# Kernel tuning notes

Measured on AMD Instinct MI355X. Metric: run time of the kernel, lower is better.

## Reference

```python
import jax, jax.numpy as jnp
import numpy as np

N, E, ND, ED, H, OUT, L, VC = 10000, 160000, 8, 4, 128, 256, 6, 6
HEADS, C = 4, 128  # GATConv: out_channels=128 per head, concat=False -> mean over heads


def _ln(x, g, b, eps=1e-5):
    m = x.mean(-1, keepdims=True)
    v = ((x - m) ** 2).mean(-1, keepdims=True)
    return (x - m) * jax.lax.rsqrt(v + eps) * g + b


def _gat_layer(h, src, dst, e_attr, lw, a_src, a_dst, lew, a_edge, bias):
    # h: [N,H]; e_attr: [Etot,H]; PyG GATConv(heads=4, concat=False, edge_dim=H)
    xh = (h @ lw).reshape(N, HEADS, C)                 # [N,4,128]
    eh = (e_attr @ lew).reshape(-1, HEADS, C)          # [Etot,4,128]
    al_s = jnp.einsum('nhc,hc->nh', xh, a_src)
    al_d = jnp.einsum('nhc,hc->nh', xh, a_dst)
    al_e = jnp.einsum('ehc,hc->eh', eh, a_edge)
    alpha = jax.nn.leaky_relu(al_s[src] + al_d[dst] + al_e, 0.2)  # [Etot,4]
    amax = jax.ops.segment_max(alpha, dst, num_segments=N)
    ex = jnp.exp(alpha - amax[dst])
    den = jax.ops.segment_sum(ex, dst, num_segments=N)
    w = ex / (den[dst] + 1e-16)
    out = jax.ops.segment_sum(xh[src] * w[..., None], dst, num_segments=N)  # [N,4,128]
    return out.mean(axis=1) + bias


def setup_inputs() -> dict:
    key = jax.random.key(0)
    ks = jax.random.split(key, 32)
    s = 0.05
    d = {
        'x': jax.random.normal(ks[0], (N, ND), jnp.float32),
        'edge_index': jax.random.randint(ks[1], (2, E), 0, N),
        'edge_attr': jax.random.uniform(ks[2], (E, ED), jnp.float32),
        'vnf_context': jax.random.normal(ks[3], (1, VC), jnp.float32),
        # node embedding
        'node_w': jax.random.normal(ks[4], (ND, H)) * s, 'node_b': jnp.zeros((H,)),
        # EdgeAttentionLayer
        'ea_proj_w': jax.random.normal(ks[5], (ED, H)) * s, 'ea_proj_b': jnp.zeros((H,)),
        'vnf_w': jax.random.normal(ks[6], (VC, H)) * s, 'vnf_b': jnp.zeros((H,)),
        'att1_w': jax.random.normal(ks[7], (2 * H, H)) * s, 'att1_b': jnp.zeros((H,)),
        'att2_w': jax.random.normal(ks[8], (H, H // 2)) * s, 'att2_b': jnp.zeros((H // 2,)),
        'att3_w': jax.random.normal(ks[9], (H // 2, 1)) * s, 'att3_b': jnp.zeros((1,)),
        # per-layer GATConv params (stacked over L layers)
        'gat_lin_w': jax.random.normal(ks[10], (L, H, HEADS * C)) * s,
        'gat_att_src': jax.random.normal(ks[11], (L, HEADS, C)) * s,
        'gat_att_dst': jax.random.normal(ks[12], (L, HEADS, C)) * s,
        'gat_lin_edge_w': jax.random.normal(ks[13], (L, H, HEADS * C)) * s,
        'gat_att_edge': jax.random.normal(ks[14], (L, HEADS, C)) * s,
        'gat_bias': jnp.zeros((L, C)),
        'ln_scale': jnp.ones((L, H)), 'ln_bias': jnp.zeros((L, H)),
        # output projection
        'out_w': jax.random.normal(ks[15], (H, OUT)) * s, 'out_b': jnp.zeros((OUT,)),
    }
    return d


def reference(x, edge_index, edge_attr, vnf_context, node_w, node_b, ea_proj_w, ea_proj_b,
              vnf_w, vnf_b, att1_w, att1_b, att2_w, att2_b, att3_w, att3_b,
              gat_lin_w, gat_att_src, gat_att_dst, gat_lin_edge_w, gat_att_edge, gat_bias,
              ln_scale, ln_bias, out_w, out_b):
    src, dst = edge_index[0], edge_index[1]
    h = x @ node_w + node_b                                   # [N,128]
    # EdgeAttentionLayer (eval mode, no network_state)
    ef = edge_attr @ ea_proj_w + ea_proj_b                    # [E,128]
    vnf = vnf_context @ vnf_w + vnf_b                         # [1,128]
    comb = jnp.concatenate([ef, jnp.broadcast_to(vnf, (E, H))], axis=-1)
    a = jax.nn.relu(comb @ att1_w + att1_b)
    a = jax.nn.relu(a @ att2_w + att2_b)
    e_gate = jax.nn.sigmoid(a @ att3_w + att3_b)              # [E,1]
    w_edge = ef * e_gate                                      # [E,128]
    # GATConv default add_self_loops=True, fill_value='mean'
    loop = jnp.arange(N)
    src2 = jnp.concatenate([src, loop])
    dst2 = jnp.concatenate([dst, loop])
    e2 = jnp.concatenate([w_edge, jnp.broadcast_to(w_edge.mean(0, keepdims=True), (N, H))], axis=0)
    for l in range(L):
        hc = _gat_layer(h, src2, dst2, e2, gat_lin_w[l], gat_att_src[l], gat_att_dst[l],
                        gat_lin_edge_w[l], gat_att_edge[l], gat_bias[l])
        h = _ln(h + jax.nn.relu(hc), ln_scale[l], ln_bias[l])
    return h @ out_w + out_b                                  # [N,256]
```

## Files before the change

### kernel.cpp

```cpp
#include <hip/hip_runtime.h>
#include <hip/hip_bf16.h>
#include <math.h>

#define Nn 10000
#define Ee 160000
#define LL 6

typedef short v8s __attribute__((ext_vector_type(8)));
typedef float v4f __attribute__((ext_vector_type(4)));

__device__ __forceinline__ unsigned short f2bf(float v) {
    unsigned int b = __float_as_uint(v);
    b += 0x7fffu + ((b >> 16) & 1u);
    return (unsigned short)(b >> 16);
}
__device__ __forceinline__ float bflo(unsigned int u) { return __uint_as_float(u << 16); }
__device__ __forceinline__ float bfhi(unsigned int u) { return __uint_as_float(u & 0xffff0000u); }

__global__ __launch_bounds__(256) void k_first(
    const float* __restrict__ x, const float* __restrict__ nw,
    const float* __restrict__ nb, float* __restrict__ h, unsigned short* __restrict__ hb,
    const int* __restrict__ ei, int* __restrict__ hist,
    const float* __restrict__ glw, const float* __restrict__ gas,
    const float* __restrict__ gad, const float* __restrict__ glew,
    const float* __restrict__ gae, float* __restrict__ Bs,
    float* __restrict__ Bd, float* __restrict__ Be,
    unsigned short* __restrict__ WsumT,
    const float* __restrict__ a2w, unsigned short* __restrict__ w2bf,
    const float* __restrict__ ow, unsigned short* __restrict__ owbT,
    const float* __restrict__ vnfc, const float* __restrict__ vw,
    const float* __restrict__ vb, const float* __restrict__ eab,
    const float* __restrict__ a1w, const float* __restrict__ a1b,
    const float* __restrict__ eaw, float* __restrict__ E1) {
    __shared__ float vr[128];
    __shared__ float sM1[512];
    __shared__ float sd1[128];
    int b = blockIdx.x, t = threadIdx.x;
    if (b < 5000) {
        int idx = b * 256 + t;
        int n = idx >> 7, c = idx & 127;
        const float* xr = x + (size_t)n * 8;
        float acc = nb[c];
#pragma unroll
        for (int k = 0; k < 8; k++) acc += xr[k] * nw[k * 128 + c];
        h[idx] = acc;
        hb[idx] = f2bf(acc);
        return;
    }
    if (b < 5625) {
        int i = (b - 5000) * 256 + t;
        atomicAdd(&hist[ei[Ee + i]], 1);
        return;
    }
    if (b < 5637) {
        int idx = (b - 5625) * 256 + t;
        if (idx >= LL * 128 * 4) return;
        int hh = idx & 3, k = (idx >> 2) & 127, l = idx >> 9;
        const float* lwp = glw  + (size_t)l * 65536 + k * 512 + hh * 128;
        const float* lep = glew + (size_t)l * 65536 + k * 512 + hh * 128;
        const float* sp = gas + l * 512 + hh * 128;
        const float* dp = gad + l * 512 + hh * 128;
        const float* ep = gae + l * 512 + hh * 128;
        float s1 = 0, s2 = 0, s3 = 0;
        for (int c = 0; c < 128; c++) {
            float lv = lwp[c];
            s1 += lv * sp[c];
            s2 += lv * dp[c];
            s3 += lep[c] * ep[c];
        }
        Bs[idx] = s1; Bd[idx] = s2; Be[idx] = s3;
        return;
    }
    if (b < 7173) {
        int idx = (b - 5637) * 256 + t;
        int kk = idx & 511;
        int c = (idx >> 9) & 127;
        int l = idx >> 16;
        float v = 0.25f * glw[(size_t)l * 65536 + (size_t)(kk & 127) * 512 + (kk >> 7) * 128 + c];
        WsumT[(size_t)l * 65536 + (size_t)c * 512 + kk] = f2bf(v);
        return;
    }
    if (b < 7205) {
        int idx = (b - 7173) * 256 + t;
        int j = idx & 7, lane = (idx >> 3) & 63, nt = (idx >> 9) & 3, ks = idx >> 11;
        int k = ks * 32 + ((lane >> 4) << 3) + j;
        int n = nt * 16 + (lane & 15);
        w2bf[idx] = f2bf(a2w[k * 64 + n]);
        return;
    }
    if (b < 7333) {
        int idx = (b - 7205) * 256 + t;
        int col = idx >> 7, kk = idx & 127;
        owbT[idx] = f2bf(ow[kk * 256 + col]);
        return;
    }
    {
        if (t < 128) {
            float a = vb[t];
#pragma unroll
            for (int k = 0; k < 6; k++) a += vnfc[k] * vw[k * 128 + t];
            vr[t] = a;
        }
        __syncthreads();
        if (t < 128) {
            float a = a1b[t];
            for (int k = 0; k < 128; k++) a += eab[k] * a1w[k * 128 + t];
            for (int k = 0; k < 128; k++) a += vr[k] * a1w[(128 + k) * 128 + t];
            sd1[t] = a;
        }
#pragma unroll
        for (int rr = 0; rr < 2; rr++) {
            int id = rr * 256 + t;
            int r = id >> 7, j = id & 127;
            float a = 0.f;
            for (int k = 0; k < 128; k++) a += eaw[r * 128 + k] * a1w[k * 128 + j];
            sM1[id] = a;
        }
        __syncthreads();
        if (t < 128) {
            E1[t * 8 + 0] = sM1[t];
            E1[t * 8 + 1] = sM1[128 + t];
            E1[t * 8 + 2] = sM1[256 + t];
            E1[t * 8 + 3] = sM1[384 + t];
            E1[t * 8 + 4] = sd1[t];
            E1[t * 8 + 5] = 0.f; E1[t * 8 + 6] = 0.f; E1[t * 8 + 7] = 0.f;
        }
    }
}

__global__ __launch_bounds__(1024) void k_scan(
    const int* __restrict__ hist, int* __restrict__ seg, int* __restrict__ pos,
    const float* __restrict__ eaw, const float* __restrict__ eab,
    const float* __restrict__ Be, float* __restrict__ PB, float* __restrict__ cB) {
    __shared__ int wsums[16];
    __shared__ int carry_s;
    int t = threadIdx.x;
    if (blockIdx.x == 1) {
        if (t >= 24) return;
        int l = t >> 2, hh = t & 3;
        const float* bp = Be + l * 512 + hh;
        float s0 = 0, s1 = 0, s2 = 0, s3 = 0, sc = 0;
        for (int k = 0; k < 128; k++) {
            float bv = bp[k * 4];
            s0 += eaw[0 * 128 + k] * bv;
            s1 += eaw[1 * 128 + k] * bv;
            s2 += eaw[2 * 128 + k] * bv;
            s3 += eaw[3 * 128 + k] * bv;
            sc += eab[k] * bv;
        }
        PB[0 * 24 + t] = s0; PB[1 * 24 + t] = s1;
        PB[2 * 24 + t] = s2; PB[3 * 24 + t] = s3;
        cB[t] = sc;
        return;
    }
    int lane = t & 63, wid = t >> 6;
    if (t == 0) { carry_s = 0; seg[0] = 0; }
    __syncthreads();
    for (int base = 0; base < Nn; base += 1024) {
        int idx = base + t;
        int v = (idx < Nn) ? hist[idx] : 0;
        int sc = v;
#pragma unroll
        for (int d = 1; d < 64; d <<= 1) {
            int up = __shfl_up(sc, d);
            if (lane >= d) sc += up;
        }
        if (lane == 63) wsums[wid] = sc;
        __syncthreads();
        if (wid == 0) {
            int wv = (lane < 16) ? wsums[lane] : 0;
            int wsc = wv;
#pragma unroll
            for (int d = 1; d < 16; d <<= 1) {
                int up = __shfl_up(wsc, d);
                if (lane >= d) wsc += up;
            }
            if (lane < 16) wsums[lane] = wsc - wv;
        }
        __syncthreads();
        int carry = carry_s;
        int inc = sc + wsums[wid] + carry;
        if (idx < Nn) { seg[idx + 1] = inc; pos[idx] = inc - v; }
        __syncthreads();
        if (t == 1023) carry_s = inc;
        __syncthreads();
    }
}

__global__ __launch_bounds__(256, 2) void k_edge(
    const float* __restrict__ ea, const float* __restrict__ E1,
    const unsigned short* __restrict__ w2bf,
    const float* __restrict__ a2b, const float* __restrict__ a3w,
    const float* __restrict__ a3b,
    const float* __restrict__ PB, const float* __restrict__ cB,
    const int* __restrict__ ei, int* __restrict__ pos, int* __restrict__ srcv,
    float* __restrict__ aleT, float* __restrict__ gsum,
    const float* __restrict__ h, const float* __restrict__ Bs,
    const float* __restrict__ Bd, float* __restrict__ als, float* __restrict__ ald) {
    __shared__ float4 sM[128];
    __shared__ float sD[128];
    __shared__ float4 sevs[256];
    __shared__ float gsh[256];
    __shared__ float sgsum[5];
    int t = threadIdx.x;
    int b = blockIdx.x;
    if (b >= 625) {
        int idx = (b - 625) * 256 + t;
        if (idx >= Nn * 8) return;
        int n = idx >> 3, slot = idx & 7;
        const float* B = (slot < 4) ? Bs : Bd;
        int hh = slot & 3;
        const float4* hr = (const float4*)(h + (size_t)n * 128);
        float s = 0.f;
#pragma unroll 8
        for (int kb = 0; kb < 32; kb++) {
            float4 hv = hr[kb];
            s += hv.x * B[(4 * kb + 0) * 4 + hh] + hv.y * B[(4 * kb + 1) * 4 + hh]
               + hv.z * B[(4 * kb + 2) * 4 + hh] + hv.w * B[(4 * kb + 3) * 4 + hh];
        }
        if (slot < 4) als[n * 4 + hh] = s;
        else          ald[n * 4 + hh] = s;
        return;
    }
    int lane = t & 63;
    int wid = t >> 6;
    int c = lane & 15, q = lane >> 4;
    int eb0 = b * 256;

    int my_src = ei[eb0 + t];
    int my_dst = ei[Ee + eb0 + t];
    sevs[t] = *(const float4*)(ea + (size_t)(eb0 + t) * 4);
    if (t < 128) {
        int slot = t ^ ((t >> 3) & 3);
        sM[slot] = *(const float4*)(E1 + t * 8);
        sD[t] = E1[t * 8 + 4];
    }
    if (t < 5) sgsum[t] = 0.f;
    __syncthreads();

    float4 ev4[4];
#pragma unroll
    for (int mt = 0; mt < 4; mt++) ev4[mt] = sevs[(wid * 4 + mt) * 16 + c];

    v8s av[4][4];
#pragma unroll
    for (int ks = 0; ks < 4; ks++) {
        float4 mr[8]; float dr[8];
#pragma unroll
        for (int j = 0; j < 8; j++) {
            int k = ks * 32 + q * 8 + j;
            mr[j] = sM[k ^ q];
            dr[j] = sD[k];
        }
#pragma unroll
        for (int mt = 0; mt < 4; mt++) {
            float4 ev = ev4[mt];
            v8s a;
#pragma unroll
            for (int j = 0; j < 8; j++) {
                float xv = fmaxf(dr[j] + ev.x * mr[j].x + ev.y * mr[j].y
                                       + ev.z * mr[j].z + ev.w * mr[j].w, 0.f);
                a[j] = (short)f2bf(xv);
            }
            av[mt][ks] = a;
        }
    }

    v4f acc[4][4];
#pragma unroll
    for (int nt = 0; nt < 4; nt++) {
        float bb = a2b[nt * 16 + c];
#pragma unroll
        for (int mt = 0; mt < 4; mt++) acc[mt][nt] = (v4f){bb, bb, bb, bb};
    }
#pragma unroll
    for (int nt = 0; nt < 4; nt++) {
#pragma unroll
        for (int ks = 0; ks < 4; ks++) {
            v8s bfr = *(const v8s*)(w2bf + ((size_t)(ks * 4 + nt) * 64 + lane) * 8);
#pragma unroll
            for (int mt = 0; mt < 4; mt++)
                acc[mt][nt] = __builtin_amdgcn_mfma_f32_16x16x32_bf16(av[mt][ks], bfr, acc[mt][nt], 0, 0, 0);
        }
    }

    float a3r[4];
#pragma unroll
    for (int nt = 0; nt < 4; nt++) a3r[nt] = a3w[nt * 16 + c];
    float a3b0 = a3b[0];
#pragma unroll
    for (int mt = 0; mt < 4; mt++) {
#pragma unroll
        for (int r = 0; r < 4; r++) {
            float s = 0.f;
#pragma unroll
            for (int nt = 0; nt < 4; nt++) s += fmaxf(acc[mt][nt][r], 0.f) * a3r[nt];
            s += __shfl_xor(s, 1); s += __shfl_xor(s, 2);
            s += __shfl_xor(s, 4); s += __shfl_xor(s, 8);
            if (c == 0) gsh[(wid * 4 + mt) * 16 + q * 4 + r] = 1.f / (1.f + __expf(-(s + a3b0)));
        }
    }
    __syncthreads();

    float g = gsh[t];
    float4 evv = sevs[t];
    float v0 = g, v1 = g * evv.x, v2 = g * evv.y, v3 = g * evv.z, v4 = g * evv.w;
#pragma unroll
    for (int d = 32; d > 0; d >>= 1) {
        v0 += __shfl_down(v0, d); v1 += __shfl_down(v1, d); v2 += __shfl_down(v2, d);
        v3 += __shfl_down(v3, d); v4 += __shfl_down(v4, d);
    }
    if (lane == 0) {
        atomicAdd(&sgsum[0], v0); atomicAdd(&sgsum[1], v1); atomicAdd(&sgsum[2], v2);
        atomicAdd(&sgsum[3], v3); atomicAdd(&sgsum[4], v4);
    }
    __syncthreads();
    if (t < 5) atomicAdd(&gsum[t], sgsum[t]);
    int slot = atomicAdd(&pos[my_dst], 1);
    srcv[slot] = my_src;
#pragma unroll
    for (int i4 = 0; i4 < 6; i4++) {
        float4 cc = *(const float4*)(cB + i4 * 4);
        float4 p0 = *(const float4*)(PB + 0 * 24 + i4 * 4);
        float4 p1 = *(const float4*)(PB + 1 * 24 + i4 * 4);
        float4 p2 = *(const float4*)(PB + 2 * 24 + i4 * 4);
        float4 p3 = *(const float4*)(PB + 3 * 24 + i4 * 4);
        float4 o;
        o.x = g * (cc.x + evv.x * p0.x + evv.y * p1.x + evv.z * p2.x + evv.w * p3.x);
        o.y = g * (cc.y + evv.x * p0.y + evv.y * p1.y + evv.z * p2.y + evv.w * p3.y);
        o.z = g * (cc.z + evv.x * p0.z + evv.y * p1.z + evv.z * p2.z + evv.w * p3.z);
        o.w = g * (cc.w + evv.x * p0.w + evv.y * p1.w + evv.z * p2.w + evv.w * p3.w);
        *(float4*)(aleT + (size_t)i4 * Ee * 4 + (size_t)slot * 4) = o;
    }
}

__global__ __launch_bounds__(256) void k_agg3(
    const int* __restrict__ srcv, const int* __restrict__ seg,
    const float* __restrict__ als, const float* __restrict__ ald,
    const float* __restrict__ aleS_l,
    const unsigned short* __restrict__ hb, unsigned short* __restrict__ aggb,
    const float* __restrict__ gsum, const float* __restrict__ PBl,
    const float* __restrict__ cBl) {
    __shared__ float part[2][512];
    __shared__ float pden[2][4];
    int t = threadIdx.x;
    int lane = t & 63;
    int wv = (t >> 6) & 1;
    int w = t >> 7;
    int n = blockIdx.x * 2 + w;
    int start = seg[n], end = seg[n + 1];
    int deg = end - start;
    int half = (deg + 1) >> 1;
    int s0 = start + wv * half;
    int e0 = wv ? end : start + half;
    int hp = lane >> 4;
    int cch = (lane & 15) * 8;
    float aldh = ald[n * 4 + hp];
    float den = 0.f;
    float4 acc0 = make_float4(0.f, 0.f, 0.f, 0.f);
    float4 acc1 = make_float4(0.f, 0.f, 0.f, 0.f);
    int i = s0;
    for (; i + 4 <= e0; i += 4) {
        int sa = srcv[i], sb = srcv[i + 1], sc = srcv[i + 2], sd = srcv[i + 3];
        float ala = aleS_l[(size_t)(i + 0) * 4 + hp];
        float alb = aleS_l[(size_t)(i + 1) * 4 + hp];
        float alc = aleS_l[(size_t)(i + 2) * 4 + hp];
        float ald_ = aleS_l[(size_t)(i + 3) * 4 + hp];
        float asa = als[sa * 4 + hp], asb = als[sb * 4 + hp];
        float asc = als[sc * 4 + hp], asd = als[sd * 4 + hp];
        uint4 ua = *(const uint4*)(hb + (size_t)sa * 128 + cch);
        uint4 ub = *(const uint4*)(hb + (size_t)sb * 128 + cch);
        uint4 uc = *(const uint4*)(hb + (size_t)sc * 128 + cch);
        uint4 ud = *(const uint4*)(hb + (size_t)sd * 128 + cch);
        float ava = asa + aldh + ala; ava = ava > 0.f ? ava : 0.2f * ava;
        float avb = asb + aldh + alb; avb = avb > 0.f ? avb : 0.2f * avb;
        float avc = asc + aldh + alc; avc = avc > 0.f ? avc : 0.2f * avc;
        float avd = asd + aldh + ald_; avd = avd > 0.f ? avd : 0.2f * avd;
        float ea = __expf(fminf(ava, 60.f));
        float eb = __expf(fminf(avb, 60.f));
        float ec = __expf(fminf(avc, 60.f));
        float ed = __expf(fminf(avd, 60.f));
        den += (ea + eb) + (ec + ed);
        acc0.x += (ea * bflo(ua.x) + eb * bflo(ub.x)) + (ec * bflo(uc.x) + ed * bflo(ud.x));
        acc0.y += (ea * bfhi(ua.x) + eb * bfhi(ub.x)) + (ec * bfhi(uc.x) + ed * bfhi(ud.x));
        acc0.z += (ea * bflo(ua.y) + eb * bflo(ub.y)) + (ec * bflo(uc.y) + ed * bflo(ud.y));
        acc0.w += (ea * bfhi(ua.y) + eb * bfhi(ub.y)) + (ec * bfhi(uc.y) + ed * bfhi(ud.y));
        acc1.x += (ea * bflo(ua.z) + eb * bflo(ub.z)) + (ec * bflo(uc.z) + ed * bflo(ud.z));
        acc1.y += (ea * bfhi(ua.z) + eb * bfhi(ub.z)) + (ec * bfhi(uc.z) + ed * bfhi(ud.z));
        acc1.z += (ea * bflo(ua.w) + eb * bflo(ub.w)) + (ec * bflo(uc.w) + ed * bflo(ud.w));
        acc1.w += (ea * bfhi(ua.w) + eb * bfhi(ub.w)) + (ec * bfhi(uc.w) + ed * bfhi(ud.w));
    }
    for (; i < e0; i++) {
        int sa = srcv[i];
        float ala = aleS_l[(size_t)i * 4 + hp];
        float ava = als[sa * 4 + hp] + aldh + ala;
        ava = ava > 0.f ? ava : 0.2f * ava;
        float ea = __expf(fminf(ava, 60.f));
        den += ea;
        uint4 ua = *(const uint4*)(hb + (size_t)sa * 128 + cch);
        acc0.x += ea * bflo(ua.x); acc0.y += ea * bfhi(ua.x);
        acc0.z += ea * bflo(ua.y); acc0.w += ea * bfhi(ua.y);
        acc1.x += ea * bflo(ua.z); acc1.y += ea * bfhi(ua.z);
        acc1.z += ea * bflo(ua.w); acc1.w += ea * bfhi(ua.w);
    }
    if (wv == 0) {
        float lale = (gsum[0] * cBl[hp] + gsum[1] * PBl[hp] + gsum[2] * PBl[24 + hp]
                    + gsum[3] * PBl[48 + hp] + gsum[4] * PBl[72 + hp]) * (1.0f / Ee);
        float av = als[n * 4 + hp] + aldh + lale;
        av = av > 0.f ? av : 0.2f * av;
        float e0 = __expf(fminf(av, 60.f));
        den += e0;
        uint4 ua = *(const uint4*)(hb + (size_t)n * 128 + cch);
        acc0.x += e0 * bflo(ua.x); acc0.y += e0 * bfhi(ua.x);
        acc0.z += e0 * bflo(ua.y); acc0.w += e0 * bfhi(ua.y);
        acc1.x += e0 * bflo(ua.z); acc1.y += e0 * bfhi(ua.z);
        acc1.z += e0 * bflo(ua.w); acc1.w += e0 * bfhi(ua.w);
    }
    if (wv == 1) {
        *(float4*)&part[w][lane * 8] = acc0;
        *(float4*)&part[w][lane * 8 + 4] = acc1;
        if ((lane & 15) == 0) pden[w][hp] = den;
    }
    __syncthreads();
    if (wv == 0) {
        float4 p0 = *(const float4*)&part[w][lane * 8];
        float4 p1 = *(const float4*)&part[w][lane * 8 + 4];
        float inv2 = 1.f / (den + pden[w][hp] + 1e-16f);
        acc0.x = (acc0.x + p0.x) * inv2; acc0.y = (acc0.y + p0.y) * inv2;
        acc0.z = (acc0.z + p0.z) * inv2; acc0.w = (acc0.w + p0.w) * inv2;
        acc1.x = (acc1.x + p1.x) * inv2; acc1.y = (acc1.y + p1.y) * inv2;
        acc1.z = (acc1.z + p1.z) * inv2; acc1.w = (acc1.w + p1.w) * inv2;
        ushort4 q0, q1;
        q0.x = f2bf(acc0.x); q0.y = f2bf(acc0.y); q0.z = f2bf(acc0.z); q0.w = f2bf(acc0.w);
        q1.x = f2bf(acc1.x); q1.y = f2bf(acc1.y); q1.z = f2bf(acc1.z); q1.w = f2bf(acc1.w);
        *(ushort4*)(aggb + (size_t)n * 512 + lane * 8) = q0;
        *(ushort4*)(aggb + (size_t)n * 512 + lane * 8 + 4) = q1;
    }
}

__global__ __launch_bounds__(256) void k_post(
    const unsigned short* __restrict__ aggb, const unsigned short* __restrict__ WsumT_l,
    const float* __restrict__ gbias, const float* __restrict__ lnsc,
    const float* __restrict__ lnbi, float* __restrict__ h,
    unsigned short* __restrict__ hb, const float* __restrict__ Bs_n,
    const float* __restrict__ Bd_n, float* __restrict__ als, float* __restrict__ ald,
    const unsigned short* __restrict__ owbT, const float* __restrict__ ob,
    float* __restrict__ out) {
    int t = threadIdx.x;
    int lane = t & 63, w = t >> 6;
    int n0 = (blockIdx.x * 4 + w) * 16;
    if (n0 >= Nn) return;
    int m = lane & 15, q = lane >> 4;
    v4f acc[8];
#pragma unroll
    for (int nt = 0; nt < 8; nt++) acc[nt] = (v4f){0.f, 0.f, 0.f, 0.f};
    const unsigned short* arow = aggb + (size_t)(n0 + m) * 512 + q * 8;
#pragma unroll 4
    for (int ks = 0; ks < 16; ks++) {
        v8s fa = *(const v8s*)(arow + ks * 32);
#pragma unroll
        for (int nt = 0; nt < 8; nt++) {
            int col = nt * 16 + m;
            v8s fb = *(const v8s*)(WsumT_l + (size_t)col * 512 + ks * 32 + q * 8);
            acc[nt] = __builtin_amdgcn_mfma_f32_16x16x32_bf16(fa, fb, acc[nt], 0, 0, 0);
        }
    }
    float v[8][4];
    float s1[4] = {0.f, 0.f, 0.f, 0.f}, s2[4] = {0.f, 0.f, 0.f, 0.f};
#pragma unroll
    for (int nt = 0; nt < 8; nt++) {
        int col = nt * 16 + m;
        float b = gbias[col];
#pragma unroll
        for (int r = 0; r < 4; r++) {
            int row = n0 + q * 4 + r;
            float val = h[(size_t)row * 128 + col] + fmaxf(acc[nt][r] + b, 0.f);
            v[nt][r] = val;
            s1[r] += val; s2[r] += val * val;
        }
    }
#pragma unroll
    for (int d = 1; d <= 8; d <<= 1) {
#pragma unroll
        for (int r = 0; r < 4; r++) {
            s1[r] += __shfl_xor(s1[r], d);
            s2[r] += __shfl_xor(s2[r], d);
        }
    }
    float o8[8][4];
#pragma unroll
    for (int r = 0; r < 4; r++) {
        float mean = s1[r] * (1.f / 128.f);
        float var = s2[r] * (1.f / 128.f) - mean * mean;
        float rinv = rsqrtf(var + 1e-5f);
        int row = n0 + q * 4 + r;
#pragma unroll
        for (int nt = 0; nt < 8; nt++) {
            int col = nt * 16 + m;
            float o = (v[nt][r] - mean) * rinv * lnsc[col] + lnbi[col];
            o8[nt][r] = o;
            h[(size_t)row * 128 + col] = o;
            hb[(size_t)row * 128 + col] = f2bf(o);
        }
    }
    if (owbT == nullptr) {
        float sal[4][4], sad[4][4];
#pragma unroll
        for (int r = 0; r < 4; r++) {
#pragma unroll
            for (int hh = 0; hh < 4; hh++) { sal[r][hh] = 0.f; sad[r][hh] = 0.f; }
        }
#pragma unroll
        for (int nt = 0; nt < 8; nt++) {
            int col = nt * 16 + m;
            float4 bs = *(const float4*)(Bs_n + col * 4);
            float4 bd = *(const float4*)(Bd_n + col * 4);
#pragma unroll
            for (int r = 0; r < 4; r++) {
                float o = o8[nt][r];
                sal[r][0] += o * bs.x; sal[r][1] += o * bs.y;
                sal[r][2] += o * bs.z; sal[r][3] += o * bs.w;
                sad[r][0] += o * bd.x; sad[r][1] += o * bd.y;
                sad[r][2] += o * bd.z; sad[r][3] += o * bd.w;
            }
        }
#pragma unroll
        for (int d = 1; d <= 8; d <<= 1) {
#pragma unroll
            for (int r = 0; r < 4; r++) {
#pragma unroll
                for (int hh = 0; hh < 4; hh++) {
                    sal[r][hh] += __shfl_xor(sal[r][hh], d);
                    sad[r][hh] += __shfl_xor(sad[r][hh], d);
                }
            }
        }
        if (m < 8) {
            int hh = m & 3;
#pragma unroll
            for (int r = 0; r < 4; r++) {
                int row = n0 + q * 4 + r;
                float va = (hh == 0) ? sal[r][0] : (hh == 1) ? sal[r][1] : (hh == 2) ? sal[r][2] : sal[r][3];
                float vd = (hh == 0) ? sad[r][0] : (hh == 1) ? sad[r][1] : (hh == 2) ? sad[r][2] : sad[r][3];
                if (m < 4) als[row * 4 + hh] = va;
                else       ald[row * 4 + hh] = vd;
            }
        }
    } else {
        v4f oacc[16];
#pragma unroll
        for (int ct = 0; ct < 16; ct++) oacc[ct] = (v4f){0.f, 0.f, 0.f, 0.f};
#pragma unroll
        for (int ks = 0; ks < 4; ks++) {
            v8s fa = *(const v8s*)(hb + (size_t)(n0 + m) * 128 + ks * 32 + q * 8);
#pragma unroll
            for (int ct = 0; ct < 16; ct++) {
                v8s fb = *(const v8s*)(owbT + (size_t)(ct * 16 + m) * 128 + ks * 32 + q * 8);
                oacc[ct] = __builtin_amdgcn_mfma_f32_16x16x32_bf16(fa, fb, oacc[ct], 0, 0, 0);
            }
        }
#pragma unroll
        for (int ct = 0; ct < 16; ct++) {
            float obv = ob[ct * 16 + m];
#pragma unroll
            for (int r = 0; r < 4; r++) {
                int row = n0 + q * 4 + r;
                out[(size_t)row * 256 + ct * 16 + m] = oacc[ct][r] + obv;
            }
        }
    }
}

extern "C" void kernel_launch(void* const* d_in, const int* in_sizes, int n_in,
                              void* d_out, int out_size, void* d_ws, size_t ws_size,
                              hipStream_t stream) {
    const float* x    = (const float*)d_in[0];
    const int*   ei   = (const int*)d_in[1];
    const float* ea   = (const float*)d_in[2];
    const float* vnfc = (const float*)d_in[3];
    const float* nw   = (const float*)d_in[4];
    const float* nb   = (const float*)d_in[5];
    const float* eaw  = (const float*)d_in[6];
    const float* eab  = (const float*)d_in[7];
    const float* vw   = (const float*)d_in[8];
    const float* vb   = (const float*)d_in[9];
    const float* a1w  = (const float*)d_in[10];
    const float* a1b  = (const float*)d_in[11];
    const float* a2w  = (const float*)d_in[12];
    const float* a2b  = (const float*)d_in[13];
    const float* a3w  = (const float*)d_in[14];
    const float* a3b  = (const float*)d_in[15];
    const float* glw  = (const float*)d_in[16];
    const float* gas  = (const float*)d_in[17];
    const float* gad  = (const float*)d_in[18];
    const float* glew = (const float*)d_in[19];
    const float* gae  = (const float*)d_in[20];
    const float* gb   = (const float*)d_in[21];
    const float* lnsc = (const float*)d_in[22];
    const float* lnbi = (const float*)d_in[23];
    const float* ow   = (const float*)d_in[24];
    const float* ob   = (const float*)d_in[25];
    float* out = (float*)d_out;

    char* w = (char*)d_ws;
    size_t o = 0;
    auto allocf = [&](size_t cnt) { float* p = (float*)(w + o); o += ((cnt * 4 + 255) / 256) * 256; return p; };
    auto alloci = [&](size_t cnt) { int* p = (int*)(w + o); o += ((cnt * 4 + 255) / 256) * 256; return p; };
    auto allocu = [&](size_t cnt) { unsigned short* p = (unsigned short*)(w + o); o += ((cnt * 2 + 255) / 256) * 256; return p; };
    int* hist     = alloci(Nn);
    float* gsum   = allocf(8);
    float* h      = allocf((size_t)Nn * 128);
    unsigned short* hb    = allocu((size_t)Nn * 128);
    unsigned short* aggb  = allocu((size_t)Nn * 512);
    unsigned short* WsumT = allocu((size_t)LL * 128 * 512);
    unsigned short* w2bf  = allocu(8192);
    unsigned short* owbT  = allocu(32768);
    float* als    = allocf((size_t)Nn * 4);
    float* ald    = allocf((size_t)Nn * 4);
    float* aleT   = allocf((size_t)LL * Ee * 4);
    float* Bs     = allocf(3072);
    float* Bd     = allocf(3072);
    float* Be     = allocf(3072);
    float* E1     = allocf(1024);
    float* PB     = allocf(96);
    float* cB     = allocf(24);
    int* seg      = alloci(Nn + 1);
    int* pos      = alloci(Nn);
    int* srcv     = alloci(Ee);

    hipMemsetAsync(hist, 0, ((size_t)Nn * 4 + 255) / 256 * 256 + 256, stream);

    k_first<<<7334, 256, 0, stream>>>(x, nw, nb, h, hb, ei, hist,
                                      glw, gas, gad, glew, gae, Bs, Bd, Be,
                                      WsumT, a2w, w2bf, ow, owbT, vnfc, vw, vb, eab,
                                      a1w, a1b, eaw, E1);
    k_scan<<<2, 1024, 0, stream>>>(hist, seg, pos, eaw, eab, Be, PB, cB);
    k_edge<<<938, 256, 0, stream>>>(ea, E1, w2bf, a2b, a3w, a3b, PB, cB,
                                    ei, pos, srcv, aleT, gsum, h, Bs, Bd, als, ald);
    for (int l = 0; l < LL; l++) {
        int ln = (l + 1) % LL;
        k_agg3<<<Nn / 2, 256, 0, stream>>>(srcv, seg, als, ald,
                                           aleT + (size_t)l * Ee * 4, hb, aggb,
                                           gsum, PB + l * 4, cB + l * 4);
        k_post<<<(625 + 3) / 4, 256, 0, stream>>>(aggb, WsumT + (size_t)l * 65536,
                                                  gb + l * 128, lnsc + l * 128, lnbi + l * 128,
                                                  h, hb, Bs + ln * 512, Bd + ln * 512, als, ald,
                                                  (l == LL - 1) ? owbT : (const unsigned short*)nullptr,
                                                  ob, out);
    }
}
```

Measured before the change: 466.1 us.

## Fuse per-layer aggregation and post-GEMM/LayerNorm into one kernel with ping-pong buffers

Merges the attention aggregation kernel and the post-aggregation GEMM/LayerNorm kernel into a single per-layer kernel. Each block aggregates 8 nodes into XOR-swizzled shared memory, and one wave then runs the MFMA projection, LayerNorm, next-layer attention logits and final output. The aggregate no longer goes through global memory, and there is one launch per layer instead of two. hb/als/ald are double-buffered so readers never see the current layer's writes. In exchange, the MFMA tiles are only half used (8 of 16 rows, rows duplicated), only one of four waves runs the GEMM epilogue, and each node's whole degree runs in one wave where it was split across two.

```diff
diff --git a/kernel.cpp b/kernel.cpp
--- a/kernel.cpp
+++ b/kernel.cpp
@@ -334,130 +334,114 @@
     }
 }
 
-__global__ __launch_bounds__(256) void k_agg3(
+__global__ __launch_bounds__(256, 4) void k_layer(
     const int* __restrict__ srcv, const int* __restrict__ seg,
-    const float* __restrict__ als, const float* __restrict__ ald,
+    const float* __restrict__ alsR, const float* __restrict__ aldR,
+    float* __restrict__ alsW, float* __restrict__ aldW,
     const float* __restrict__ aleS_l,
-    const unsigned short* __restrict__ hb, unsigned short* __restrict__ aggb,
+    const unsigned short* __restrict__ hbR, unsigned short* __restrict__ hbW,
     const float* __restrict__ gsum, const float* __restrict__ PBl,
-    const float* __restrict__ cBl) {
-    __shared__ float part[2][512];
-    __shared__ float pden[2][4];
+    const float* __restrict__ cBl,
+    const unsigned short* __restrict__ WsumT_l, const float* __restrict__ gbias,
+    const float* __restrict__ lnsc_l, const float* __restrict__ lnbi_l,
+    float* __restrict__ h, const float* __restrict__ Bs_n,
+    const float* __restrict__ Bd_n,
+    const unsigned short* __restrict__ owbT, const float* __restrict__ ob,
+    float* __restrict__ out) {
+    __shared__ unsigned short aggs[8 * 512];
     int t = threadIdx.x;
-    int lane = t & 63;
-    int wv = (t >> 6) & 1;
-    int w = t >> 7;
-    int n = blockIdx.x * 2 + w;
-    int start = seg[n], end = seg[n + 1];
-    int deg = end - start;
-    int half = (deg + 1) >> 1;
-    int s0 = start + wv * half;
-    int e0 = wv ? end : start + half;
+    int lane = t & 63, w = t >> 6;
+    int n0 = blockIdx.x * 8;
     int hp = lane >> 4;
     int cch = (lane & 15) * 8;
-    float aldh = ald[n * 4 + hp];
-    float den = 0.f;
-    float4 acc0 = make_float4(0.f, 0.f, 0.f, 0.f);
-    float4 acc1 = make_float4(0.f, 0.f, 0.f, 0.f);
-    int i = s0;
-    for (; i + 4 <= e0; i += 4) {
-        int sa = srcv[i], sb = srcv[i + 1], sc = srcv[i + 2], sd = srcv[i + 3];
-        float ala = aleS_l[(size_t)(i + 0) * 4 + hp];
-        float alb = aleS_l[(size_t)(i + 1) * 4 + hp];
-        float alc = aleS_l[(size_t)(i + 2) * 4 + hp];
-        float ald_ = aleS_l[(size_t)(i + 3) * 4 + hp];
-        float asa = als[sa * 4 + hp], asb = als[sb * 4 + hp];
-        float asc = als[sc * 4 + hp], asd = als[sd * 4 + hp];
-        uint4 ua = *(const uint4*)(hb + (size_t)sa * 128 + cch);
-        uint4 ub = *(const uint4*)(hb + (size_t)sb * 128 + cch);
-        uint4 uc = *(const uint4*)(hb + (size_t)sc * 128 + cch);
-        uint4 ud = *(const uint4*)(hb + (size_t)sd * 128 + cch);
-        float ava = asa + aldh + ala; ava = ava > 0.f ? ava : 0.2f * ava;
-        float avb = asb + aldh + alb; avb = avb > 0.f ? avb : 0.2f * avb;
-        float avc = asc + aldh + alc; avc = avc > 0.f ? avc : 0.2f * avc;
-        float avd = asd + aldh + ald_; avd = avd > 0.f ? avd : 0.2f * avd;
-        float ea = __expf(fminf(ava, 60.f));
-        float eb = __expf(fminf(avb, 60.f));
-        float ec = __expf(fminf(avc, 60.f));
-        float ed = __expf(fminf(avd, 60.f));
-        den += (ea + eb) + (ec + ed);
-        acc0.x += (ea * bflo(ua.x) + eb * bflo(ub.x)) + (ec * bflo(uc.x) + ed * bflo(ud.x));
-        acc0.y += (ea * bfhi(ua.x) + eb * bfhi(ub.x)) + (ec * bfhi(uc.x) + ed * bfhi(ud.x));
-        acc0.z += (ea * bflo(ua.y) + eb * bflo(ub.y)) + (ec * bflo(uc.y) + ed * bflo(ud.y));
-        acc0.w += (ea * bfhi(ua.y) + eb * bfhi(ub.y)) + (ec * bfhi(uc.y) + ed * bfhi(ud.y));
-        acc1.x += (ea * bflo(ua.z) + eb * bflo(ub.z)) + (ec * bflo(uc.z) + ed * bflo(ud.z));
-        acc1.y += (ea * bfhi(ua.z) + eb * bfhi(ub.z)) + (ec * bfhi(uc.z) + ed * bfhi(ud.z));
-        acc1.z += (ea * bflo(ua.w) + eb * bflo(ub.w)) + (ec * bflo(uc.w) + ed * bflo(ud.w));
-        acc1.w += (ea * bfhi(ua.w) + eb * bfhi(ub.w)) + (ec * bfhi(uc.w) + ed * bfhi(ud.w));
-    }
-    for (; i < e0; i++) {
-        int sa = srcv[i];
-        float ala = aleS_l[(size_t)i * 4 + hp];
-        float ava = als[sa * 4 + hp] + aldh + ala;
-        ava = ava > 0.f ? ava : 0.2f * ava;
-        float ea = __expf(fminf(ava, 60.f));
-        den += ea;
-        uint4 ua = *(const uint4*)(hb + (size_t)sa * 128 + cch);
-        acc0.x += ea * bflo(ua.x); acc0.y += ea * bfhi(ua.x);
-        acc0.z += ea * bflo(ua.y); acc0.w += ea * bfhi(ua.y);
-        acc1.x += ea * bflo(ua.z); acc1.y += ea * bfhi(ua.z);
-        acc1.z += ea * bflo(ua.w); acc1.w += ea * bfhi(ua.w);
-    }
-    if (wv == 0) {
-        float lale = (gsum[0] * cBl[hp] + gsum[1] * PBl[hp] + gsum[2] * PBl[24 + hp]
-                    + gsum[3] * PBl[48 + hp] + gsum[4] * PBl[72 + hp]) * (1.0f / Ee);
-        float av = als[n * 4 + hp] + aldh + lale;
-        av = av > 0.f ? av : 0.2f * av;
-        float e0 = __expf(fminf(av, 60.f));
-        den += e0;
-        uint4 ua = *(const uint4*)(hb + (size_t)n * 128 + cch);
-        acc0.x += e0 * bflo(ua.x); acc0.y += e0 * bfhi(ua.x);
-        acc0.z += e0 * bflo(ua.y); acc0.w += e0 * bfhi(ua.y);
-        acc1.x += e0 * bflo(ua.z); acc1.y += e0 * bfhi(ua.z);
-        acc1.z += e0 * bflo(ua.w); acc1.w += e0 * bfhi(ua.w);
-    }
-    if (wv == 1) {
-        *(float4*)&part[w][lane * 8] = acc0;
-        *(float4*)&part[w][lane * 8 + 4] = acc1;
-        if ((lane & 15) == 0) pden[w][hp] = den;
+    float lale = (gsum[0] * cBl[hp] + gsum[1] * PBl[hp] + gsum[2] * PBl[24 + hp]
+                + gsum[3] * PBl[48 + hp] + gsum[4] * PBl[72 + hp]) * (1.0f / Ee);
+
+    for (int nn = 0; nn < 2; nn++) {
+        int mrow = w * 2 + nn;
+        int n = n0 + mrow;
+        int start = seg[n], end = seg[n + 1];
+        float aldh = aldR[n * 4 + hp];
+        float den = 0.f;
+        float4 acc0 = make_float4(0.f, 0.f, 0.f, 0.f);
+        float4 acc1 = make_float4(0.f, 0.f, 0.f, 0.f);
+        int i = start;
+        for (; i + 4 <= end; i += 4) {
+            int sa = srcv[i], sb = srcv[i + 1], sc = srcv[i + 2], sd = srcv[i + 3];
+            float ala = aleS_l[(size_t)(i + 0) * 4 + hp];
+            float alb = aleS_l[(size_t)(i + 1) * 4 + hp];
+            float alc = aleS_l[(size_t)(i + 2) * 4 + hp];
+            float ald_ = aleS_l[(size_t)(i + 3) * 4 + hp];
+            float asa = alsR[sa * 4 + hp], asb = alsR[sb * 4 + hp];
+            float asc = alsR[sc * 4 + hp], asd = alsR[sd * 4 + hp];
+            uint4 ua = *(const uint4*)(hbR + (size_t)sa * 128 + cch);
+            uint4 ub = *(const uint4*)(hbR + (size_t)sb * 128 + cch);
+            uint4 uc = *(const uint4*)(hbR + (size_t)sc * 128 + cch);
+            uint4 ud = *(const uint4*)(hbR + (size_t)sd * 128 + cch);
+            float ava = asa + aldh + ala; ava = ava > 0.f ? ava : 0.2f * ava;
+            float avb = asb + aldh + alb; avb = avb > 0.f ? avb : 0.2f * avb;
+            float avc = asc + aldh + alc; avc = avc > 0.f ? avc : 0.2f * avc;
+            float avd = asd + aldh + ald_; avd = avd > 0.f ? avd : 0.2f * avd;
+            float ea = __expf(fminf(ava, 60.f));
+            float eb = __expf(fminf(avb, 60.f));
+            float ec = __expf(fminf(avc, 60.f));
+            float ed = __expf(fminf(avd, 60.f));
+            den += (ea + eb) + (ec + ed);
+            acc0.x += (ea * bflo(ua.x) + eb * bflo(ub.x)) + (ec * bflo(uc.x) + ed * bflo(ud.x));
+            acc0.y += (ea * bfhi(ua.x) + eb * bfhi(ub.x)) + (ec * bfhi(uc.x) + ed * bfhi(ud.x));
+            acc0.z += (ea * bflo(ua.y) + eb * bflo(ub.y)) + (ec * bflo(uc.y) + ed * bflo(ud.y));
+            acc0.w += (ea * bfhi(ua.y) + eb * bfhi(ub.y)) + (ec * bfhi(uc.y) + ed * bfhi(ud.y));
+            acc1.x += (ea * bflo(ua.z) + eb * bflo(ub.z)) + (ec * bflo(uc.z) + ed * bflo(ud.z));
+            acc1.y += (ea * bfhi(ua.z) + eb * bfhi(ub.z)) + (ec * bfhi(uc.z) + ed * bfhi(ud.z));
+            acc1.z += (ea * bflo(ua.w) + eb * bflo(ub.w)) + (ec * bflo(uc.w) + ed * bflo(ud.w));
+            acc1.w += (ea * bfhi(ua.w) + eb * bfhi(ub.w)) + (ec * bfhi(uc.w) + ed * bfhi(ud.w));
+        }
+        for (; i < end; i++) {
+            int sa = srcv[i];
+            float ala = aleS_l[(size_t)i * 4 + hp];
+            float ava = alsR[sa * 4 + hp] + aldh + ala;
+            ava = ava > 0.f ? ava : 0.2f * ava;
+            float ea = __expf(fminf(ava, 60.f));
+            den += ea;
+            uint4 ua = *(const uint4*)(hbR + (size_t)sa * 128 + cch);
+            acc0.x += ea * bflo(ua.x); acc0.y += ea * bfhi(ua.x);
+            acc0.z += ea * bflo(ua.y); acc0.w += ea * bfhi(ua.y);
+            acc1.x += ea * bflo(ua.z); acc1.y += ea * bfhi(ua.z);
+            acc1.z += ea * bflo(ua.w); acc1.w += ea * bfhi(ua.w);
+        }
+        {
+            float av = alsR[n * 4 + hp] + aldh + lale;
+            av = av > 0.f ? av : 0.2f * av;
+            float e0 = __expf(fminf(av, 60.f));
+            den += e0;
+            uint4 ua = *(const uint4*)(hbR + (size_t)n * 128 + cch);
+            acc0.x += e0 * bflo(ua.x); acc0.y += e0 * bfhi(ua.x);
+            acc0.z += e0 * bflo(ua.y); acc0.w += e0 * bfhi(ua.y);
+            acc1.x += e0 * bflo(ua.z); acc1.y += e0 * bfhi(ua.z);
+            acc1.z += e0 * bflo(ua.w); acc1.w += e0 * bfhi(ua.w);
+        }
+        float inv2 = 1.f / (den + 1e-16f);
+        ushort4 pk0, pk1;
+        pk0.x = f2bf(acc0.x * inv2); pk0.y = f2bf(acc0.y * inv2);
+        pk0.z = f2bf(acc0.z * inv2); pk0.w = f2bf(acc0.w * inv2);
+        pk1.x = f2bf(acc1.x * inv2); pk1.y = f2bf(acc1.y * inv2);
+        pk1.z = f2bf(acc1.z * inv2); pk1.w = f2bf(acc1.w * inv2);
+        int fi = mrow * 512 + ((lane * 8) ^ (mrow << 3));
+        *(ushort4*)(aggs + fi) = pk0;
+        *(ushort4*)(aggs + fi + 4) = pk1;
     }
     __syncthreads();
-    if (wv == 0) {
-        float4 p0 = *(const float4*)&part[w][lane * 8];
-        float4 p1 = *(const float4*)&part[w][lane * 8 + 4];
-        float inv2 = 1.f / (den + pden[w][hp] + 1e-16f);
-        acc0.x = (acc0.x + p0.x) * inv2; acc0.y = (acc0.y + p0.y) * inv2;
-        acc0.z = (acc0.z + p0.z) * inv2; acc0.w = (acc0.w + p0.w) * inv2;
-        acc1.x = (acc1.x + p1.x) * inv2; acc1.y = (acc1.y + p1.y) * inv2;
-        acc1.z = (acc1.z + p1.z) * inv2; acc1.w = (acc1.w + p1.w) * inv2;
-        ushort4 q0, q1;
-        q0.x = f2bf(acc0.x); q0.y = f2bf(acc0.y); q0.z = f2bf(acc0.z); q0.w = f2bf(acc0.w);
-        q1.x = f2bf(acc1.x); q1.y = f2bf(acc1.y); q1.z = f2bf(acc1.z); q1.w = f2bf(acc1.w);
-        *(ushort4*)(aggb + (size_t)n * 512 + lane * 8) = q0;
-        *(ushort4*)(aggb + (size_t)n * 512 + lane * 8 + 4) = q1;
-    }
-}
-
-__global__ __launch_bounds__(256) void k_post(
-    const unsigned short* __restrict__ aggb, const unsigned short* __restrict__ WsumT_l,
-    const float* __restrict__ gbias, const float* __restrict__ lnsc,
-    const float* __restrict__ lnbi, float* __restrict__ h,
-    unsigned short* __restrict__ hb, const float* __restrict__ Bs_n,
-    const float* __restrict__ Bd_n, float* __restrict__ als, float* __restrict__ ald,
-    const unsigned short* __restrict__ owbT, const float* __restrict__ ob,
-    float* __restrict__ out) {
-    int t = threadIdx.x;
-    int lane = t & 63, w = t >> 6;
-    int n0 = (blockIdx.x * 4 + w) * 16;
-    if (n0 >= Nn) return;
+    if (w != 0) return;
+
     int m = lane & 15, q = lane >> 4;
+    int mm = m & 7;
     v4f acc[8];
 #pragma unroll
     for (int nt = 0; nt < 8; nt++) acc[nt] = (v4f){0.f, 0.f, 0.f, 0.f};
-    const unsigned short* arow = aggb + (size_t)(n0 + m) * 512 + q * 8;
 #pragma unroll 4
     for (int ks = 0; ks < 16; ks++) {
-        v8s fa = *(const v8s*)(arow + ks * 32);
+        int fi = mm * 512 + ((ks * 32 + q * 8) ^ (mm << 3));
+        v8s fa = *(const v8s*)(aggs + fi);
 #pragma unroll
         for (int nt = 0; nt < 8; nt++) {
             int col = nt * 16 + m;
@@ -473,7 +457,7 @@
         float b = gbias[col];
 #pragma unroll
         for (int r = 0; r < 4; r++) {
-            int row = n0 + q * 4 + r;
+            int row = n0 + ((q * 4 + r) & 7);
             float val = h[(size_t)row * 128 + col] + fmaxf(acc[nt][r] + b, 0.f);
             v[nt][r] = val;
             s1[r] += val; s2[r] += val * val;
@@ -493,14 +477,16 @@
         float mean = s1[r] * (1.f / 128.f);
         float var = s2[r] * (1.f / 128.f) - mean * mean;
         float rinv = rsqrtf(var + 1e-5f);
-        int row = n0 + q * 4 + r;
+        int row = n0 + ((q * 4 + r) & 7);
 #pragma unroll
         for (int nt = 0; nt < 8; nt++) {
             int col = nt * 16 + m;
-            float o = (v[nt][r] - mean) * rinv * lnsc[col] + lnbi[col];
+            float o = (v[nt][r] - mean) * rinv * lnsc_l[col] + lnbi_l[col];
             o8[nt][r] = o;
-            h[(size_t)row * 128 + col] = o;
-            hb[(size_t)row * 128 + col] = f2bf(o);
+            if (q < 2) {
+                h[(size_t)row * 128 + col] = o;
+                hbW[(size_t)row * 128 + col] = f2bf(o);
+            }
         }
     }
     if (owbT == nullptr) {
@@ -535,37 +521,44 @@
                 }
             }
         }
-        if (m < 8) {
+        if (m < 8 && q < 2) {
             int hh = m & 3;
 #pragma unroll
             for (int r = 0; r < 4; r++) {
                 int row = n0 + q * 4 + r;
                 float va = (hh == 0) ? sal[r][0] : (hh == 1) ? sal[r][1] : (hh == 2) ? sal[r][2] : sal[r][3];
                 float vd = (hh == 0) ? sad[r][0] : (hh == 1) ? sad[r][1] : (hh == 2) ? sad[r][2] : sad[r][3];
-                if (m < 4) als[row * 4 + hh] = va;
-                else       ald[row * 4 + hh] = vd;
+                if (m < 4) alsW[row * 4 + hh] = va;
+                else       aldW[row * 4 + hh] = vd;
             }
         }
     } else {
-        v4f oacc[16];
-#pragma unroll
-        for (int ct = 0; ct < 16; ct++) oacc[ct] = (v4f){0.f, 0.f, 0.f, 0.f};
-#pragma unroll
-        for (int ks = 0; ks < 4; ks++) {
-            v8s fa = *(const v8s*)(hb + (size_t)(n0 + m) * 128 + ks * 32 + q * 8);
-#pragma unroll
-            for (int ct = 0; ct < 16; ct++) {
-                v8s fb = *(const v8s*)(owbT + (size_t)(ct * 16 + m) * 128 + ks * 32 + q * 8);
-                oacc[ct] = __builtin_amdgcn_mfma_f32_16x16x32_bf16(fa, fb, oacc[ct], 0, 0, 0);
-            }
-        }
-#pragma unroll
-        for (int ct = 0; ct < 16; ct++) {
-            float obv = ob[ct * 16 + m];
-#pragma unroll
-            for (int r = 0; r < 4; r++) {
-                int row = n0 + q * 4 + r;
-                out[(size_t)row * 256 + ct * 16 + m] = oacc[ct][r] + obv;
+#pragma unroll
+        for (int g = 0; g < 4; g++) {
+            v4f oacc[4];
+#pragma unroll
+            for (int ci = 0; ci < 4; ci++) oacc[ci] = (v4f){0.f, 0.f, 0.f, 0.f};
+#pragma unroll
+            for (int ks = 0; ks < 4; ks++) {
+                v8s fa = *(const v8s*)(hbW + (size_t)(n0 + mm) * 128 + ks * 32 + q * 8);
+#pragma unroll
+                for (int ci = 0; ci < 4; ci++) {
+                    int ct = g * 4 + ci;
+                    v8s fb = *(const v8s*)(owbT + (size_t)(ct * 16 + m) * 128 + ks * 32 + q * 8);
+                    oacc[ci] = __builtin_amdgcn_mfma_f32_16x16x32_bf16(fa, fb, oacc[ci], 0, 0, 0);
+                }
+            }
+            if (q < 2) {
+#pragma unroll
+                for (int ci = 0; ci < 4; ci++) {
+                    int ct = g * 4 + ci;
+                    float obv = ob[ct * 16 + m];
+#pragma unroll
+                    for (int r = 0; r < 4; r++) {
+                        int row = n0 + q * 4 + r;
+                        out[(size_t)row * 256 + ct * 16 + m] = oacc[ci][r] + obv;
+                    }
+                }
             }
         }
     }
@@ -610,13 +603,15 @@
     int* hist     = alloci(Nn);
     float* gsum   = allocf(8);
     float* h      = allocf((size_t)Nn * 128);
-    unsigned short* hb    = allocu((size_t)Nn * 128);
-    unsigned short* aggb  = allocu((size_t)Nn * 512);
+    unsigned short* hb0   = allocu((size_t)Nn * 128);
+    unsigned short* hb1   = allocu((size_t)Nn * 128);
     unsigned short* WsumT = allocu((size_t)LL * 128 * 512);
     unsigned short* w2bf  = allocu(8192);
     unsigned short* owbT  = allocu(32768);
-    float* als    = allocf((size_t)Nn * 4);
-    float* ald    = allocf((size_t)Nn * 4);
+    float* als0   = allocf((size_t)Nn * 4);
+    float* ald0   = allocf((size_t)Nn * 4);
+    float* als1   = allocf((size_t)Nn * 4);
+    float* ald1   = allocf((size_t)Nn * 4);
     float* aleT   = allocf((size_t)LL * Ee * 4);
     float* Bs     = allocf(3072);
     float* Bd     = allocf(3072);
@@ -630,22 +625,28 @@
 
     hipMemsetAsync(hist, 0, ((size_t)Nn * 4 + 255) / 256 * 256 + 256, stream);
 
-    k_first<<<7334, 256, 0, stream>>>(x, nw, nb, h, hb, ei, hist,
+    k_first<<<7334, 256, 0, stream>>>(x, nw, nb, h, hb0, ei, hist,
                                       glw, gas, gad, glew, gae, Bs, Bd, Be,
                                       WsumT, a2w, w2bf, ow, owbT, vnfc, vw, vb, eab,
                                       a1w, a1b, eaw, E1);
     k_scan<<<2, 1024, 0, stream>>>(hist, seg, pos, eaw, eab, Be, PB, cB);
     k_edge<<<938, 256, 0, stream>>>(ea, E1, w2bf, a2b, a3w, a3b, PB, cB,
-                                    ei, pos, srcv, aleT, gsum, h, Bs, Bd, als, ald);
+                                    ei, pos, srcv, aleT, gsum, h, Bs, Bd, als0, ald0);
     for (int l = 0; l < LL; l++) {
+        const float* alsR = (l & 1) ? als1 : als0;
+        const float* aldR = (l & 1) ? ald1 : ald0;
+        float* alsW = (l & 1) ? als0 : als1;
+        float* aldW = (l & 1) ? ald0 : ald1;
+        const unsigned short* hbR = (l & 1) ? hb1 : hb0;
+        unsigned short* hbW = (l & 1) ? hb0 : hb1;
         int ln = (l + 1) % LL;
-        k_agg3<<<Nn / 2, 256, 0, stream>>>(srcv, seg, als, ald,
-                                           aleT + (size_t)l * Ee * 4, hb, aggb,
-                                           gsum, PB + l * 4, cB + l * 4);
-        k_post<<<(625 + 3) / 4, 256, 0, stream>>>(aggb, WsumT + (size_t)l * 65536,
-                                                  gb + l * 128, lnsc + l * 128, lnbi + l * 128,
-                                                  h, hb, Bs + ln * 512, Bd + ln * 512, als, ald,
-                                                  (l == LL - 1) ? owbT : (const unsigned short*)nullptr,
-                                                  ob, out);
+        k_layer<<<1250, 256, 0, stream>>>(srcv, seg, alsR, aldR, alsW, aldW,
+                                          aleT + (size_t)l * Ee * 4, hbR, hbW,
+                                          gsum, PB + l * 4, cB + l * 4,
+                                          WsumT + (size_t)l * 65536, gb + l * 128,
+                                          lnsc + l * 128, lnbi + l * 128,
+                                          h, Bs + ln * 512, Bd + ln * 512,
+                                          (l == LL - 1) ? owbT : (const unsigned short*)nullptr,
+                                          ob, out);
     }
 }
```

New measurement: 491.3 us. 1.05x slower.
